# Optimization experiments

Measured on AMD Instinct MI355X. Metric: run time of the kernel, lower is better.

## Reference

```python
import jax, jax.numpy as jnp
import numpy as np

N_FFT = 2048
HOP = 441
WIN_SIZE = 7
PAD = WIN_SIZE // 2
NP_WIN = WIN_SIZE * WIN_SIZE
COV_NORM = NP_WIN / (NP_WIN - 1.0)  # sample covariance, skimage default
DATA_RANGE = 2.0  # skimage float dtype_range (-1,1)
C1 = (0.01 * DATA_RANGE) ** 2
C2 = (0.03 * DATA_RANGE) ** 2
EPS = 1e-8

# periodic hann window (librosa fftbins=True)
_HANN = 0.5 - 0.5 * np.cos(2.0 * np.pi * np.arange(N_FFT) / N_FFT)


def wav_to_spectrogram(x):
    # x: [B, C, S] -> magnitude spectrogram [B, C, T, F]
    pad = N_FFT // 2
    xp = jnp.pad(x, ((0, 0), (0, 0), (pad, pad)), mode='reflect')  # torch 'reflect'
    L = xp.shape[-1]
    n_frames = (L - N_FFT) // HOP + 1
    idx = jnp.arange(n_frames)[:, None] * HOP + jnp.arange(N_FFT)[None, :]
    frames = xp[..., idx] * jnp.asarray(_HANN, xp.dtype)  # [B,C,T,N_FFT]
    spec = jnp.fft.rfft(frames, axis=-1)
    mag = jnp.sqrt(jnp.maximum(spec.real ** 2 + spec.imag ** 2, EPS))
    return mag


def _umean_last(x):
    # 1D uniform mean filter (size 7) along last axis, scipy 'reflect' boundary
    xp = jnp.pad(x, [(0, 0)] * (x.ndim - 1) + [(PAD, PAD)], mode='symmetric')
    cs = jnp.cumsum(xp, axis=-1)
    zero = jnp.zeros(cs.shape[:-1] + (1,), cs.dtype)
    cs = jnp.concatenate([zero, cs], axis=-1)
    return (cs[..., WIN_SIZE:] - cs[..., :-WIN_SIZE]) / WIN_SIZE


def umean2d(x):
    # separable 7x7 uniform filter over last two axes
    x = _umean_last(x)
    x = jnp.swapaxes(_umean_last(jnp.swapaxes(x, -1, -2)), -1, -2)
    return x


def ssim_map_mean(X, Y):
    ux, uy = umean2d(X), umean2d(Y)
    uxx, uyy, uxy = umean2d(X * X), umean2d(Y * Y), umean2d(X * Y)
    vx = COV_NORM * (uxx - ux * ux)
    vy = COV_NORM * (uyy - uy * uy)
    vxy = COV_NORM * (uxy - ux * uy)
    S = ((2 * ux * uy + C1) * (2 * vxy + C2)) / ((ux * ux + uy * uy + C1) * (vx + vy + C2))
    # crop pad on each side (skimage) then mean over the spatial map
    return jnp.mean(S[..., PAD:-PAD, PAD:-PAD], axis=(-2, -1))


def setup_inputs() -> dict:
    key = jax.random.key(0)
    k1, k2 = jax.random.split(key)
    B, C, S = 32, 2, 176400
    output = jax.random.normal(k1, (B, C, S), dtype=jnp.float32)
    target = jax.random.normal(k2, (B, C, S), dtype=jnp.float32)
    return {"output": output, "target": target}


def reference(output, target):
    so = wav_to_spectrogram(output)
    st = wav_to_spectrogram(target)
    res = ssim_map_mean(so, st)  # [B, C]
    return res[..., None, None]  # [B, C, 1, 1]
```

## Files before the change

kernel.cpp:

```cpp
#include <hip/hip_runtime.h>
#include <math.h>

#ifndef M_PI
#define M_PI 3.14159265358979323846
#endif

constexpr int S_LEN    = 176400;
constexpr int NFFT     = 2048;
constexpr int NC       = 1024;
constexpr int HOP_     = 441;
constexpr int T_FRAMES = 401;
constexpr int F_BINS   = 1025;
constexpr int F_STRIDE = 1028;
constexpr int N_CH     = 64;
constexpr float EPS_   = 1e-8f;
constexpr float C1_    = 0.0004f;
constexpr float C2_    = 0.0036f;
constexpr float COV_NORM_ = 49.0f / 48.0f;

constexpr int WIN_OFF  = 0;
constexpr int TWG_OFF  = 2048;
constexpr int UTW_OFF  = 3584;
constexpr int SPEC_OFF = 5696;

constexpr int ROWS_PW   = 24;
constexpr int NCHUNKS_R = 17;
constexpr int BANDS     = 5;
constexpr int BAND_ADV  = 248;

__device__ __forceinline__ int phys(int i) { return i ^ ((i >> 2) & 15) ^ ((i >> 6) & 15); }

__device__ __forceinline__ float2 cadd(float2 a, float2 b){ return make_float2(a.x+b.x, a.y+b.y); }
__device__ __forceinline__ float2 csub(float2 a, float2 b){ return make_float2(a.x-b.x, a.y-b.y); }
__device__ __forceinline__ float2 cmul(float2 a, float2 b){ return make_float2(a.x*b.x-a.y*b.y, a.x*b.y+a.y*b.x); }

__global__ __launch_bounds__(256) void init_tables_kernel(float* __restrict__ ws, float* __restrict__ out) {
    const int idx = blockIdx.x * 256 + threadIdx.x;
    if (idx < 64) out[idx] = 0.0f;
    if (idx < NFFT) {
        ws[WIN_OFF + idx] = 0.5f - 0.5f * cosf((float)(2.0 * M_PI / NFFT) * (float)idx);
    }
    if (idx < 768) {
        float ang = -2.0f * (float)M_PI * (float)idx / (float)NC;
        float s, c; sincosf(ang, &s, &c);
        ws[TWG_OFF + 2*idx] = c; ws[TWG_OFF + 2*idx+1] = s;
    }
    if (idx < F_BINS) {
        float ang = -(float)M_PI * (float)idx / (float)NC;
        float s, c; sincosf(ang, &s, &c);
        ws[UTW_OFF + 2*idx] = c; ws[UTW_OFF + 2*idx+1] = s;
    }
}

__device__ __forceinline__ void r4_dif_inplace(
    float2* __restrict__ A, int r0, int r1, int r2, int r3,
    float2 w1, float2 w2, float2 w3, bool tw)
{
    float2 x0c = A[r0];
    float2 x1c = A[r1];
    float2 x2c = A[r2];
    float2 x3c = A[r3];

    float2 a = cadd(x0c, x2c);
    float2 b = csub(x0c, x2c);
    float2 c = cadd(x1c, x3c);
    float2 d = csub(x1c, x3c);

    float2 y0 = cadd(a, c);
    float2 y2 = csub(a, c);
    float2 y1 = make_float2(b.x + d.y, b.y - d.x);
    float2 y3 = make_float2(b.x - d.y, b.y + d.x);

    A[r0] = y0;
    A[r1] = tw ? cmul(y1, w1) : y1;
    A[r2] = tw ? cmul(y2, w2) : y2;
    A[r3] = tw ? cmul(y3, w3) : y3;
}

__global__ __launch_bounds__(256, 8) void stft_mag_kernel(
    const float* __restrict__ x0, const float* __restrict__ x1,
    float* __restrict__ ws, int ch0, int nch, int swizzle)
{
    __shared__ float2 buf[2 * NC];

    const int tid = threadIdx.x;

    int ch, t;
    if (swizzle) {
        int g = blockIdx.x;
        ch = ch0 + (g & 7) * 8 + ((g >> 3) & 7);
        t  = g >> 6;
    } else {
        t  = blockIdx.x;
        ch = ch0 + blockIdx.y;
    }

    const float* __restrict__ xin0 = x0 + (size_t)ch * S_LEN;
    const float* __restrict__ xin1 = x1 + (size_t)ch * S_LEN;
    const float*  __restrict__ win = ws + WIN_OFF;
    const float2* __restrict__ twg = (const float2*)(ws + TWG_OFF);
    const float2* __restrict__ utw = (const float2*)(ws + UTW_OFF);

    const int base = t * HOP_ - NFFT / 2;
    float* fA0 = (float*)buf;
    float* fA1 = (float*)(buf + NC);
    if (base >= 0 && base + NFFT <= S_LEN) {
        #pragma unroll
        for (int k = 0; k < NFFT / 256; ++k) {
            int n = k * 256 + tid;
            int j = base + n;
            float w = win[n];
            int p = 2 * phys(n >> 1) + (n & 1);
            fA0[p] = xin0[j] * w;
            fA1[p] = xin1[j] * w;
        }
    } else {
        #pragma unroll
        for (int k = 0; k < NFFT / 256; ++k) {
            int n = k * 256 + tid;
            int j = base + n;
            j = (j < 0) ? -j : j;
            j = (j >= S_LEN) ? (2 * S_LEN - 2 - j) : j;
            float w = win[n];
            int p = 2 * phys(n >> 1) + (n & 1);
            fA0[p] = xin0[j] * w;
            fA1[p] = xin1[j] * w;
        }
    }
    __syncthreads();

    #pragma unroll
    for (int s = 0; s < 5; ++s) {
        const int M  = 256 >> (2 * s);
        const int q  = tid & (M - 1);
        const int e  = q << (2 * s);
        const int i0 = 4 * (tid - q) + q;

        const int r0 = phys(i0);
        const int r1 = phys(i0 + M);
        const int r2 = phys(i0 + 2 * M);
        const int r3 = phys(i0 + 3 * M);

        float2 w1, w2, w3;
        if (s < 4) {
            w1 = twg[e];
            w2 = twg[2 * e];
            w3 = twg[3 * e];
        } else {
            w1 = w2 = w3 = make_float2(1.0f, 0.0f);
        }

        r4_dif_inplace(buf,      r0, r1, r2, r3, w1, w2, w3, s < 4);
        r4_dif_inplace(buf + NC, r0, r1, r2, r3, w1, w2, w3, s < 4);

        __syncthreads();
    }

    const size_t perT = (size_t)T_FRAMES * F_STRIDE;
    float* __restrict__ sout0 =
        ws + SPEC_OFF + (size_t)(ch - ch0) * perT + (size_t)t * F_STRIDE;
    float* __restrict__ sout1 = sout0 + (size_t)nch * perT;

    const int R8 = ((tid & 3) << 6) | ((tid & 12) << 2) | ((tid >> 2) & 12) | ((tid >> 6) & 3);

    #pragma unroll
    for (int k = 0; k < 5; ++k) {
        int r = k * 256 + tid;
        if (k < 4 || tid == 0) {
            const int ra = (k < 4) ? ((R8 << 2) | k) : 0;
            const int rn = (NC - r) & (NC - 1);
            const int rb = ((rn & 3) << 8) | ((rn & 12) << 4) | (rn & 48)
                         | ((rn >> 4) & 12) | ((rn >> 8) & 3);
            const int ia = phys(ra);
            const int ib = phys(rb);
            float2 wu = utw[r];

            {
                float2 Zr = buf[ia];
                float2 Zn = buf[ib];
                float Ex = 0.5f * (Zr.x + Zn.x);
                float Ey = 0.5f * (Zr.y - Zn.y);
                float Ox = 0.5f * (Zr.y + Zn.y);
                float Oy = 0.5f * (Zn.x - Zr.x);
                float Xx = Ex + wu.x * Ox - wu.y * Oy;
                float Xy = Ey + wu.x * Oy + wu.y * Ox;
                sout0[r] = sqrtf(fmaxf(Xx * Xx + Xy * Xy, EPS_));
            }
            {
                float2 Zr = buf[NC + ia];
                float2 Zn = buf[NC + ib];
                float Ex = 0.5f * (Zr.x + Zn.x);
                float Ey = 0.5f * (Zr.y - Zn.y);
                float Ox = 0.5f * (Zr.y + Zn.y);
                float Oy = 0.5f * (Zn.x - Zr.x);
                float Xx = Ex + wu.x * Ox - wu.y * Oy;
                float Xy = Ey + wu.x * Oy + wu.y * Ox;
                sout1[r] = sqrtf(fmaxf(Xx * Xx + Xy * Xy, EPS_));
            }
        }
    }
}

#define HWIN7(sarr, W) {                                                     \
    float p0 = sarr[0], p01 = p0 + sarr[1], p012 = p01 + sarr[2],            \
          P = p012 + sarr[3];                                                \
    float a1 = __shfl_down(p012, 1, 64);                                     \
    float A1 = __shfl_down(P,    1, 64);                                     \
    float b0 = __shfl_down(p0,   2, 64);                                     \
    float b1 = __shfl_down(p01,  2, 64);                                     \
    W[0] = P + a1;                                                           \
    W[1] = P - p0 + A1;                                                      \
    W[2] = W[1] - sarr[1] + b0;                                              \
    W[3] = W[2] - sarr[2] + (b1 - b0);                                       \
}

__global__ __launch_bounds__(256) void ssim_kernel(
    const float* __restrict__ ws, float* __restrict__ out,
    int ch0, int nch)
{
    const int tid  = threadIdx.x;
    const int wid  = blockIdx.x * 4 + (tid >> 6);
    const int lane = tid & 63;
    const int total = nch * BANDS * NCHUNKS_R;
    if (wid >= total) return;

    const int cg    = wid / (BANDS * NCHUNKS_R);
    const int rem   = wid - cg * (BANDS * NCHUNKS_R);
    const int band  = rem / NCHUNKS_R;
    const int chunk = rem - band * NCHUNKS_R;

    const int t0 = 3 + chunk * ROWS_PW;
    const int t1 = min(t0 + ROWS_PW, T_FRAMES - 3);

    const int cb = band * BAND_ADV;
    int c4 = cb + 4 * lane;
    if (c4 > 1024) c4 = 1024;

    const size_t perT = (size_t)T_FRAMES * F_STRIDE;
    const float* __restrict__ X = ws + SPEC_OFF + (size_t)cg * perT + c4;
    const float* __restrict__ Y = ws + SPEC_OFF + ((size_t)nch + cg) * perT + c4;

    const int  fo      = cb + 3 + 4 * lane;
    const bool lane_ok = (lane <= 61);
    const float inv49  = 1.0f / 49.0f;

    float sx[4] = {0,0,0,0}, sy[4] = {0,0,0,0}, sxx[4] = {0,0,0,0},
          syy[4] = {0,0,0,0}, sxy[4] = {0,0,0,0};
    float rgx[6][4], rgy[6][4];

    #pragma unroll
    for (int w = 0; w < 6; ++w) {
        const int rr = t0 - 3 + w;
        float4 xv = *(const float4*)(X + (size_t)rr * F_STRIDE);
        float4 yv = *(const float4*)(Y + (size_t)rr * F_STRIDE);
        float xa[4] = {xv.x, xv.y, xv.z, xv.w}, ya[4] = {yv.x, yv.y, yv.z, yv.w};
        #pragma unroll
        for (int c = 0; c < 4; ++c) {
            sx[c] += xa[c]; sy[c] += ya[c];
            sxx[c] += xa[c]*xa[c]; syy[c] += ya[c]*ya[c]; sxy[c] += xa[c]*ya[c];
            rgx[w][c] = xa[c]; rgy[w][c] = ya[c];
        }
    }

    float4 cxa = *(const float4*)(X + (size_t)(t0 + 3) * F_STRIDE);
    float4 cya = *(const float4*)(Y + (size_t)(t0 + 3) * F_STRIDE);

    double acc = 0.0;

    #pragma unroll 1
    for (int tb = t0; tb < t1; tb += 6) {
        #pragma unroll
        for (int j = 0; j < 6; ++j) {
            const int t = tb + j;
            const int tn = min(t + 4, T_FRAMES - 1);
            float4 nxa = *(const float4*)(X + (size_t)tn * F_STRIDE);
            float4 nya = *(const float4*)(Y + (size_t)tn * F_STRIDE);

            float xa[4] = {cxa.x, cxa.y, cxa.z, cxa.w};
            float ya[4] = {cya.x, cya.y, cya.z, cya.w};

            #pragma unroll
            for (int c = 0; c < 4; ++c) {
                sx[c] += xa[c]; sy[c] += ya[c];
                sxx[c] += xa[c]*xa[c]; syy[c] += ya[c]*ya[c]; sxy[c] += xa[c]*ya[c];
            }

            float wx[4], wy[4], wxx[4], wyy[4], wxy[4];
            HWIN7(sx,  wx);
            HWIN7(sy,  wy);
            HWIN7(sxx, wxx);
            HWIN7(syy, wyy);
            HWIN7(sxy, wxy);

            const bool live = (t < t1);
            #pragma unroll
            for (int c = 0; c < 4; ++c) {
                if (live && lane_ok && (fo + c <= 1021)) {
                    float ux  = wx[c]  * inv49, uy  = wy[c]  * inv49;
                    float uxx = wxx[c] * inv49, uyy = wyy[c] * inv49, uxy = wxy[c] * inv49;
                    float vx  = COV_NORM_ * (uxx - ux * ux);
                    float vy  = COV_NORM_ * (uyy - uy * uy);
                    float vxy = COV_NORM_ * (uxy - ux * uy);
                    float Sv = ((2.f * ux * uy + C1_) * (2.f * vxy + C2_)) /
                               ((ux * ux + uy * uy + C1_) * (vx + vy + C2_));
                    acc += (double)Sv;
                }
            }

            #pragma unroll
            for (int c = 0; c < 4; ++c) {
                float bx_ = rgx[j][c], by_ = rgy[j][c];
                sx[c]  -= bx_;      sy[c]  -= by_;
                sxx[c] -= bx_*bx_;  syy[c] -= by_*by_;  sxy[c] -= bx_*by_;
                rgx[j][c] = xa[c];  rgy[j][c] = ya[c];
            }

            cxa = nxa; cya = nya;
        }
    }

    #pragma unroll
    for (int off = 32; off > 0; off >>= 1) acc += __shfl_down(acc, off, 64);
    if (lane == 0) {
        atomicAdd(&out[ch0 + cg], (float)(acc / (395.0 * 1019.0)));
    }
}

extern "C" void kernel_launch(void* const* d_in, const int* in_sizes, int n_in,
                              void* d_out, int out_size, void* d_ws, size_t ws_size,
                              hipStream_t stream) {
    const float* x0 = (const float*)d_in[0];
    const float* x1 = (const float*)d_in[1];
    float* out = (float*)d_out;
    float* ws  = (float*)d_ws;

    const size_t table_bytes  = (size_t)SPEC_OFF * sizeof(float);
    const size_t per_ch_bytes = (size_t)2 * T_FRAMES * F_STRIDE * sizeof(float);
    int G = (int)((ws_size - table_bytes) / per_ch_bytes);
    if (G > N_CH) G = N_CH;
    if (G < 1)    G = 1;

    init_tables_kernel<<<dim3(16), dim3(256), 0, stream>>>(ws, out);

    for (int ch0 = 0; ch0 < N_CH; ch0 += G) {
        const int nch = (N_CH - ch0 < G) ? (N_CH - ch0) : G;

        if (nch == 64) {
            stft_mag_kernel<<<dim3(T_FRAMES * 64), dim3(256), 0, stream>>>(x0, x1, ws, ch0, nch, 1);
        } else {
            stft_mag_kernel<<<dim3(T_FRAMES, nch), dim3(256), 0, stream>>>(x0, x1, ws, ch0, nch, 0);
        }

        const int nwaves = nch * BANDS * NCHUNKS_R;
        ssim_kernel<<<dim3((nwaves + 3) / 4), dim3(256), 0, stream>>>(ws, out, ch0, nch);
    }
}
```

Measured before the change: 344.1 us.

## Use packed FP32 inline asm for radix-4 butterflies and split STFT launch

Replaces the float2 complex add/sub/mul in the radix-4 DIF butterflies with hand-written v_pk_add_f32, v_pk_mul_f32 and v_pk_fma_f32 inline assembly, using op_sel and neg modifiers for the multiply-by-i and twiddle products. This aims to halve the VALU instruction count of the FFT stages. It also drops the swizzled block-to-channel mapping and, when the workspace holds all channels, launches the STFT as two 2D grids of 32 channels each before one SSIM kernel. Inline asm prevents compiler scheduling around those ops, and losing the swizzle may change L2 locality of input reads.

```diff
diff --git a/kernel.cpp b/kernel.cpp
--- a/kernel.cpp
+++ b/kernel.cpp
@@ -28,11 +28,32 @@
 constexpr int BANDS     = 5;
 constexpr int BAND_ADV  = 248;
 
+typedef float vf2 __attribute__((ext_vector_type(2)));
+
 __device__ __forceinline__ int phys(int i) { return i ^ ((i >> 2) & 15) ^ ((i >> 6) & 15); }
 
-__device__ __forceinline__ float2 cadd(float2 a, float2 b){ return make_float2(a.x+b.x, a.y+b.y); }
-__device__ __forceinline__ float2 csub(float2 a, float2 b){ return make_float2(a.x-b.x, a.y-b.y); }
-__device__ __forceinline__ float2 cmul(float2 a, float2 b){ return make_float2(a.x*b.x-a.y*b.y, a.x*b.y+a.y*b.x); }
+__device__ __forceinline__ vf2 pk_add(vf2 a, vf2 b) {
+    vf2 r; asm("v_pk_add_f32 %0, %1, %2" : "=v"(r) : "v"(a), "v"(b)); return r;
+}
+__device__ __forceinline__ vf2 pk_sub(vf2 a, vf2 b) {
+    vf2 r; asm("v_pk_add_f32 %0, %1, %2 neg_lo:[0,1] neg_hi:[0,1]" : "=v"(r) : "v"(a), "v"(b)); return r;
+}
+__device__ __forceinline__ vf2 pk_sub_i(vf2 b, vf2 d) {
+    vf2 r; asm("v_pk_add_f32 %0, %1, %2 op_sel:[0,1] op_sel_hi:[1,0] neg_hi:[0,1]"
+               : "=v"(r) : "v"(b), "v"(d)); return r;
+}
+__device__ __forceinline__ vf2 pk_add_i(vf2 b, vf2 d) {
+    vf2 r; asm("v_pk_add_f32 %0, %1, %2 op_sel:[0,1] op_sel_hi:[1,0] neg_lo:[0,1]"
+               : "=v"(r) : "v"(b), "v"(d)); return r;
+}
+__device__ __forceinline__ vf2 pk_cmul(vf2 y, vf2 w) {
+    vf2 t, r;
+    asm("v_pk_mul_f32 %0, %1, %2 op_sel:[0,0] op_sel_hi:[0,1]"
+        : "=v"(t) : "v"(y), "v"(w));
+    asm("v_pk_fma_f32 %0, %1, %2, %3 op_sel:[1,1,0] op_sel_hi:[1,0,1] neg_lo:[1,0,0]"
+        : "=v"(r) : "v"(y), "v"(w), "v"(t));
+    return r;
+}
 
 __global__ __launch_bounds__(256) void init_tables_kernel(float* __restrict__ ws, float* __restrict__ out) {
     const int idx = blockIdx.x * 256 + threadIdx.x;
@@ -53,53 +74,45 @@
 }
 
 __device__ __forceinline__ void r4_dif_inplace(
-    float2* __restrict__ A, int r0, int r1, int r2, int r3,
-    float2 w1, float2 w2, float2 w3, bool tw)
+    vf2* __restrict__ A, int r0, int r1, int r2, int r3,
+    vf2 w1, vf2 w2, vf2 w3, bool tw)
 {
-    float2 x0c = A[r0];
-    float2 x1c = A[r1];
-    float2 x2c = A[r2];
-    float2 x3c = A[r3];
-
-    float2 a = cadd(x0c, x2c);
-    float2 b = csub(x0c, x2c);
-    float2 c = cadd(x1c, x3c);
-    float2 d = csub(x1c, x3c);
-
-    float2 y0 = cadd(a, c);
-    float2 y2 = csub(a, c);
-    float2 y1 = make_float2(b.x + d.y, b.y - d.x);
-    float2 y3 = make_float2(b.x - d.y, b.y + d.x);
+    vf2 x0c = A[r0];
+    vf2 x1c = A[r1];
+    vf2 x2c = A[r2];
+    vf2 x3c = A[r3];
+
+    vf2 a = pk_add(x0c, x2c);
+    vf2 b = pk_sub(x0c, x2c);
+    vf2 c = pk_add(x1c, x3c);
+    vf2 d = pk_sub(x1c, x3c);
+
+    vf2 y0 = pk_add(a, c);
+    vf2 y2 = pk_sub(a, c);
+    vf2 y1 = pk_sub_i(b, d);
+    vf2 y3 = pk_add_i(b, d);
 
     A[r0] = y0;
-    A[r1] = tw ? cmul(y1, w1) : y1;
-    A[r2] = tw ? cmul(y2, w2) : y2;
-    A[r3] = tw ? cmul(y3, w3) : y3;
+    A[r1] = tw ? pk_cmul(y1, w1) : y1;
+    A[r2] = tw ? pk_cmul(y2, w2) : y2;
+    A[r3] = tw ? pk_cmul(y3, w3) : y3;
 }
 
 __global__ __launch_bounds__(256, 8) void stft_mag_kernel(
     const float* __restrict__ x0, const float* __restrict__ x1,
-    float* __restrict__ ws, int ch0, int nch, int swizzle)
+    float* __restrict__ ws, int ch0, int chbase, int nlay)
 {
-    __shared__ float2 buf[2 * NC];
+    __shared__ vf2 buf[2 * NC];
 
     const int tid = threadIdx.x;
-
-    int ch, t;
-    if (swizzle) {
-        int g = blockIdx.x;
-        ch = ch0 + (g & 7) * 8 + ((g >> 3) & 7);
-        t  = g >> 6;
-    } else {
-        t  = blockIdx.x;
-        ch = ch0 + blockIdx.y;
-    }
+    const int t   = blockIdx.x;
+    const int ch  = ch0 + blockIdx.y;
 
     const float* __restrict__ xin0 = x0 + (size_t)ch * S_LEN;
     const float* __restrict__ xin1 = x1 + (size_t)ch * S_LEN;
-    const float*  __restrict__ win = ws + WIN_OFF;
-    const float2* __restrict__ twg = (const float2*)(ws + TWG_OFF);
-    const float2* __restrict__ utw = (const float2*)(ws + UTW_OFF);
+    const float* __restrict__ win  = ws + WIN_OFF;
+    const vf2*   __restrict__ twg  = (const vf2*)(ws + TWG_OFF);
+    const vf2*   __restrict__ utw  = (const vf2*)(ws + UTW_OFF);
 
     const int base = t * HOP_ - NFFT / 2;
     float* fA0 = (float*)buf;
@@ -141,13 +154,13 @@
         const int r2 = phys(i0 + 2 * M);
         const int r3 = phys(i0 + 3 * M);
 
-        float2 w1, w2, w3;
+        vf2 w1, w2, w3;
         if (s < 4) {
             w1 = twg[e];
             w2 = twg[2 * e];
             w3 = twg[3 * e];
         } else {
-            w1 = w2 = w3 = make_float2(1.0f, 0.0f);
+            w1.x = 1.0f; w1.y = 0.0f; w2 = w1; w3 = w1;
         }
 
         r4_dif_inplace(buf,      r0, r1, r2, r3, w1, w2, w3, s < 4);
@@ -158,8 +171,8 @@
 
     const size_t perT = (size_t)T_FRAMES * F_STRIDE;
     float* __restrict__ sout0 =
-        ws + SPEC_OFF + (size_t)(ch - ch0) * perT + (size_t)t * F_STRIDE;
-    float* __restrict__ sout1 = sout0 + (size_t)nch * perT;
+        ws + SPEC_OFF + (size_t)(ch - chbase) * perT + (size_t)t * F_STRIDE;
+    float* __restrict__ sout1 = sout0 + (size_t)nlay * perT;
 
     const int R8 = ((tid & 3) << 6) | ((tid & 12) << 2) | ((tid >> 2) & 12) | ((tid >> 6) & 3);
 
@@ -173,11 +186,11 @@
                          | ((rn >> 4) & 12) | ((rn >> 8) & 3);
             const int ia = phys(ra);
             const int ib = phys(rb);
-            float2 wu = utw[r];
+            vf2 wu = utw[r];
 
             {
-                float2 Zr = buf[ia];
-                float2 Zn = buf[ib];
+                vf2 Zr = buf[ia];
+                vf2 Zn = buf[ib];
                 float Ex = 0.5f * (Zr.x + Zn.x);
                 float Ey = 0.5f * (Zr.y - Zn.y);
                 float Ox = 0.5f * (Zr.y + Zn.y);
@@ -187,8 +200,8 @@
                 sout0[r] = sqrtf(fmaxf(Xx * Xx + Xy * Xy, EPS_));
             }
             {
-                float2 Zr = buf[NC + ia];
-                float2 Zn = buf[NC + ib];
+                vf2 Zr = buf[NC + ia];
+                vf2 Zn = buf[NC + ib];
                 float Ex = 0.5f * (Zr.x + Zn.x);
                 float Ey = 0.5f * (Zr.y - Zn.y);
                 float Ox = 0.5f * (Zr.y + Zn.y);
@@ -342,16 +355,17 @@
 
     init_tables_kernel<<<dim3(16), dim3(256), 0, stream>>>(ws, out);
 
-    for (int ch0 = 0; ch0 < N_CH; ch0 += G) {
-        const int nch = (N_CH - ch0 < G) ? (N_CH - ch0) : G;
-
-        if (nch == 64) {
-            stft_mag_kernel<<<dim3(T_FRAMES * 64), dim3(256), 0, stream>>>(x0, x1, ws, ch0, nch, 1);
-        } else {
-            stft_mag_kernel<<<dim3(T_FRAMES, nch), dim3(256), 0, stream>>>(x0, x1, ws, ch0, nch, 0);
-        }
-
-        const int nwaves = nch * BANDS * NCHUNKS_R;
-        ssim_kernel<<<dim3((nwaves + 3) / 4), dim3(256), 0, stream>>>(ws, out, ch0, nch);
-    }
-}
+    if (G >= N_CH) {
+        stft_mag_kernel<<<dim3(T_FRAMES, 32), dim3(256), 0, stream>>>(x0, x1, ws,  0, 0, N_CH);
+        stft_mag_kernel<<<dim3(T_FRAMES, 32), dim3(256), 0, stream>>>(x0, x1, ws, 32, 0, N_CH);
+        const int nwaves = N_CH * BANDS * NCHUNKS_R;
+        ssim_kernel<<<dim3((nwaves + 3) / 4), dim3(256), 0, stream>>>(ws, out, 0, N_CH);
+    } else {
+        for (int ch0 = 0; ch0 < N_CH; ch0 += G) {
+            const int nch = (N_CH - ch0 < G) ? (N_CH - ch0) : G;
+            stft_mag_kernel<<<dim3(T_FRAMES, nch), dim3(256), 0, stream>>>(x0, x1, ws, ch0, ch0, nch);
+            const int nwaves = nch * BANDS * NCHUNKS_R;
+            ssim_kernel<<<dim3((nwaves + 3) / 4), dim3(256), 0, stream>>>(ws, out, ch0, nch);
+        }
+    }
+}
```

Result: slower. 351.2 us (+2.1%).
